# Kernel optimization log

Measured on AMD Instinct MI355X. Metric: run time of the kernel, lower is better.

## Reference

```python
import jax, jax.numpy as jnp
import numpy as np

B, V, D, H = 16, 20000, 256, 256
EPS = 1e-5


def _ln(x, g, b):
    m = jnp.mean(x, axis=-1, keepdims=True)
    v = jnp.mean(jnp.square(x - m), axis=-1, keepdims=True)
    return (x - m) * jax.lax.rsqrt(v + EPS) * g + b


def setup_inputs() -> dict:
    key = jax.random.key(0)
    ks = jax.random.split(key, 8)
    s = 1.0 / np.sqrt(D)
    return {
        "patient_emb": jax.random.normal(ks[0], (B, D), jnp.float32),
        "atc4_emb_matrix": jax.random.normal(ks[1], (V, D), jnp.float32),
        "Wp": jax.random.normal(ks[2], (D, D), jnp.float32) * s,
        "bp": jnp.zeros((D,), jnp.float32),
        "gp": jnp.ones((D,), jnp.float32),
        "betap": jnp.zeros((D,), jnp.float32),
        "Wa": jax.random.normal(ks[3], (D, D), jnp.float32) * s,
        "ba": jnp.zeros((D,), jnp.float32),
        "ga": jnp.ones((D,), jnp.float32),
        "betaa": jnp.zeros((D,), jnp.float32),
        "W1": jax.random.normal(ks[4], (2 * D, H), jnp.float32) * (1.0 / np.sqrt(2 * D)),
        "b1": jnp.zeros((H,), jnp.float32),
        "W2": jax.random.normal(ks[5], (H,), jnp.float32) * (1.0 / np.sqrt(H)),
        "b2": jnp.zeros((1,), jnp.float32),
        "g_pred": jnp.ones((V,), jnp.float32),
        "b_pred": jnp.zeros((V,), jnp.float32),
    }


def reference(patient_emb, atc4_emb_matrix, Wp, bp, gp, betap, Wa, ba, ga, betaa,
              W1, b1, W2, b2, g_pred, b_pred):
    # patient projector + layernorm: (B, D)
    p = _ln(patient_emb @ Wp + bp, gp, betap)
    # atc4 projector + layernorm: (V, D)
    a = _ln(atc4_emb_matrix @ Wa + ba, ga, betaa)
    # AttentionFusion: concat([p_expand, a_expand], -1) @ W1 == p@W1[:D] + a@W1[D:]
    ph = p @ W1[:D]            # (B, H)
    ah = a @ W1[D:]            # (V, H)
    h = jnp.tanh(ph[:, None, :] + ah[None, :, :] + b1)   # (B, V, H)
    scores = jnp.einsum('bvh,h->bv', h, W2) + b2[0]       # (B, V)
    # pred layernorm over the vocab dimension
    return _ln(scores, g_pred, b_pred)
```

## Files before the change

kernel.cpp:

```cpp
#include <hip/hip_runtime.h>


typedef unsigned short ushort_t;
typedef __attribute__((ext_vector_type(8))) short short8;
typedef __attribute__((ext_vector_type(4))) float floatx4;

#define C2F 2.8853900817779268f
#define V_N 20000
#define NBLK 1250

__device__ __forceinline__ ushort_t f2bf(float f) {
    unsigned int u = __builtin_bit_cast(unsigned int, f);
    u += 0x7FFFu + ((u >> 16) & 1u);
    return (ushort_t)(u >> 16);
}
__device__ __forceinline__ float exp2_fast(float x) { return __builtin_amdgcn_exp2f(x); }
__device__ __forceinline__ float rcp_fast(float x)  { return __builtin_amdgcn_rcpf(x); }

__global__ __launch_bounds__(1024) void prep_kernel(
    const float* __restrict__ patient_emb, const float* __restrict__ Wp,
    const float* __restrict__ bp, const float* __restrict__ gp,
    const float* __restrict__ betap, const float* __restrict__ Wa,
    const float* __restrict__ W1, ushort_t* __restrict__ pWa,
    ushort_t* __restrict__ pW1b, float* __restrict__ EpT)
{
    const int blk = blockIdx.x;
    const int tid = threadIdx.x;
    __shared__ float peL[256];
    __shared__ float pL[256];
    __shared__ float part[4][256];
    __shared__ float red[8];

    if (blk < 16) {
        int slot = blk * 1024 + tid;
        int matrix = slot >> 13;
        int rest = slot & 8191;
        int s = rest >> 10, T = (rest >> 6) & 15, l = rest & 63;
        const float* src = matrix ? (W1 + 256 * 256) : Wa;
        ushort_t* dst = matrix ? pW1b : pWa;
        int kbase = s * 32 + ((l >> 4) << 3);
        int nn = (T << 4) + (l & 15);
        short8 t;
        #pragma unroll
        for (int j = 0; j < 8; ++j)
            t[j] = (short)f2bf(src[(kbase + j) * 256 + nn]);
        *(short8*)(dst + rest * 8) = t;
        return;
    }

    const int b = blk - 16;
    const int j = tid & 255, pq = tid >> 8;
    if (tid < 256) peL[tid] = patient_emb[b * 256 + tid];
    __syncthreads();
    float a0 = 0.f;
    #pragma unroll 8
    for (int dd = 0; dd < 64; ++dd) {
        int d = pq * 64 + dd;
        a0 += peL[d] * Wp[d * 256 + j];
    }
    part[pq][j] = a0;
    __syncthreads();
    float x = 0.f;
    if (tid < 256) {
        x = part[0][j] + part[1][j] + part[2][j] + part[3][j] + bp[j];
        float s1 = x, s2 = x * x;
        #pragma unroll
        for (int off = 32; off; off >>= 1) {
            s1 += __shfl_xor(s1, off);
            s2 += __shfl_xor(s2, off);
        }
        int wv = tid >> 6;
        if ((tid & 63) == 0) { red[wv * 2] = s1; red[wv * 2 + 1] = s2; }
    }
    __syncthreads();
    if (tid < 256) {
        float s1 = red[0] + red[2] + red[4] + red[6];
        float s2 = red[1] + red[3] + red[5] + red[7];
        float mean = s1 * (1.f / 256.f);
        float var  = s2 * (1.f / 256.f) - mean * mean;
        float rstd = rsqrtf(var + 1e-5f);
        pL[tid] = (x - mean) * rstd * gp[tid] + betap[tid];
    }
    __syncthreads();
    float a2 = 0.f;
    #pragma unroll 8
    for (int dd = 0; dd < 64; ++dd) {
        int d = pq * 64 + dd;
        a2 += pL[d] * W1[d * 256 + j];
    }
    part[pq][j] = a2;
    __syncthreads();
    if (tid < 256)
        EpT[tid * 16 + b] = exp2_fast(
            C2F * (part[0][tid] + part[1][tid] + part[2][tid] + part[3][tid]));
}

__global__ __launch_bounds__(256, 3) void mega_kernel(
    const float* __restrict__ atc4, const float* __restrict__ ba,
    const float* __restrict__ ga, const float* __restrict__ betaa,
    const float* __restrict__ b1, const float* __restrict__ W2,
    const ushort_t* __restrict__ pWa, const ushort_t* __restrict__ pW1b,
    const float* __restrict__ EpT, float* __restrict__ scores,
    float* __restrict__ s1g, float* __restrict__ s2g)
{
    __shared__ ushort_t AtileF[4096];
    __shared__ float EpL[256 * 20];
    __shared__ float statsP[4][16][2];
    __shared__ float statsF[16][2];
    __shared__ float redbuf[16][4][17];

    const int tid = threadIdx.x;
    const int w = tid >> 6, lane = tid & 63;
    const int q = lane >> 4, n = lane & 15;
    const int v0 = blockIdx.x * 16;

    #pragma unroll
    for (int i = 0; i < 16; ++i) {
        int idx = i * 256 + tid;
        EpL[(idx >> 4) * 20 + (idx & 15)] = EpT[idx];
    }
    {
        const int row = tid >> 4;
        const int kb = (tid & 15) * 16;
        const float* srcp = atc4 + (v0 + row) * 256 + kb;
        #pragma unroll
        for (int i = 0; i < 4; ++i) {
            int k = kb + i * 4;
            float4 f = *(const float4*)(srcp + i * 4);
            ushort4 usv = make_ushort4(f2bf(f.x), f2bf(f.y), f2bf(f.z), f2bf(f.w));
            int addr = (((k >> 5) * 64) + (((k >> 3) & 3) * 16) + row) * 8 + (k & 7);
            *(ushort4*)(AtileF + addr) = usv;
        }
    }
    __syncthreads();

    floatx4 acc[4];
    #pragma unroll
    for (int ni = 0; ni < 4; ++ni) acc[ni] = (floatx4){0.f, 0.f, 0.f, 0.f};
    #pragma unroll
    for (int s = 0; s < 8; ++s) {
        short8 a0 = ((const short8*)AtileF)[s * 64 + lane];
        #pragma unroll
        for (int ni = 0; ni < 4; ++ni) {
            short8 bfv = *(const short8*)(pWa + ((s * 16 + w * 4 + ni) * 64 + lane) * 8);
            acc[ni] = __builtin_amdgcn_mfma_f32_16x16x32_bf16(a0, bfv, acc[ni], 0, 0, 0);
        }
    }

    float bac[4], gac[4], bec[4], b1c[4], w2c[4];
    #pragma unroll
    for (int ni = 0; ni < 4; ++ni) {
        int col = w * 64 + ni * 16 + n;
        bac[ni] = ba[col]; gac[ni] = ga[col]; bec[ni] = betaa[col];
        b1c[ni] = C2F * b1[col]; w2c[ni] = W2[col];
    }

    float s1v[4] = {0, 0, 0, 0}, s2v[4] = {0, 0, 0, 0};
    #pragma unroll
    for (int ni = 0; ni < 4; ++ni)
        #pragma unroll
        for (int r = 0; r < 4; ++r) {
            float x = acc[ni][r] + bac[ni];
            acc[ni][r] = x;
            s1v[r] += x; s2v[r] += x * x;
        }
    #pragma unroll
    for (int off = 1; off < 16; off <<= 1)
        #pragma unroll
        for (int r = 0; r < 4; ++r) {
            s1v[r] += __shfl_xor(s1v[r], off);
            s2v[r] += __shfl_xor(s2v[r], off);
        }
    if (n == 0) {
        #pragma unroll
        for (int r = 0; r < 4; ++r) {
            statsP[w][q * 4 + r][0] = s1v[r];
            statsP[w][q * 4 + r][1] = s2v[r];
        }
    }
    __syncthreads();
    if (tid < 16) {
        float m1 = statsP[0][tid][0] + statsP[1][tid][0] + statsP[2][tid][0] + statsP[3][tid][0];
        float m2 = statsP[0][tid][1] + statsP[1][tid][1] + statsP[2][tid][1] + statsP[3][tid][1];
        float mean = m1 * (1.f / 256.f);
        float var  = m2 * (1.f / 256.f) - mean * mean;
        statsF[tid][0] = mean;
        statsF[tid][1] = rsqrtf(var + 1e-5f);
    }
    __syncthreads();

    #pragma unroll
    for (int r = 0; r < 4; ++r) {
        int row = q * 4 + r;
        float mean = statsF[row][0], rstd = statsF[row][1];
        #pragma unroll
        for (int ni = 0; ni < 4; ++ni) {
            float xv = (acc[ni][r] - mean) * rstd * gac[ni] + bec[ni];
            int addr = ((w * 2 + (ni >> 1)) * 64 +
                        ((ni & 1) * 2 + (n >> 3)) * 16 + row) * 8 + (n & 7);
            AtileF[addr] = f2bf(xv);
        }
    }
    __syncthreads();

    floatx4 acc2[4];
    #pragma unroll
    for (int ni = 0; ni < 4; ++ni) acc2[ni] = (floatx4){0.f, 0.f, 0.f, 0.f};
    #pragma unroll
    for (int s = 0; s < 8; ++s) {
        short8 a0 = ((const short8*)AtileF)[s * 64 + lane];
        #pragma unroll
        for (int ni = 0; ni < 4; ++ni) {
            short8 bfv = *(const short8*)(pW1b + ((s * 16 + w * 4 + ni) * 64 + lane) * 8);
            acc2[ni] = __builtin_amdgcn_mfma_f32_16x16x32_bf16(a0, bfv, acc2[ni], 0, 0, 0);
        }
    }

    #pragma unroll
    for (int ni = 0; ni < 4; ++ni)
        #pragma unroll
        for (int r = 0; r < 4; ++r)
            acc2[ni][r] = exp2_fast(fmaf(C2F, acc2[ni][r], b1c[ni]));

    #pragma unroll 1
    for (int p = 0; p < 4; ++p) {
        float accs[4][4];
        #pragma unroll
        for (int bb = 0; bb < 4; ++bb)
            #pragma unroll
            for (int r = 0; r < 4; ++r) accs[bb][r] = 0.f;
        #pragma unroll
        for (int ni = 0; ni < 4; ++ni) {
            int base = (w * 64 + ni * 16 + n) * 20 + p * 4;
            float4 e0 = *(const float4*)(&EpL[base]);
            float ep[4] = {e0.x, e0.y, e0.z, e0.w};
            #pragma unroll
            for (int bb = 0; bb < 4; ++bb)
                #pragma unroll
                for (int r = 0; r < 4; ++r)
                    accs[bb][r] += w2c[ni] * rcp_fast(fmaf(ep[bb], acc2[ni][r], 1.f));
        }
        float t2v[2][4], t1[4];
        {
            int hb = n & 1;
            #pragma unroll
            for (int p2 = 0; p2 < 2; ++p2)
                #pragma unroll
                for (int r = 0; r < 4; ++r) {
                    float keep = hb ? accs[2 * p2 + 1][r] : accs[2 * p2][r];
                    float send = hb ? accs[2 * p2][r] : accs[2 * p2 + 1][r];
                    t2v[p2][r] = keep + __shfl_xor(send, 1);
                }
            hb = (n >> 1) & 1;
            #pragma unroll
            for (int r = 0; r < 4; ++r) {
                float keep = hb ? t2v[1][r] : t2v[0][r];
                float send = hb ? t2v[0][r] : t2v[1][r];
                t1[r] = keep + __shfl_xor(send, 2);
            }
            #pragma unroll
            for (int r = 0; r < 4; ++r) {
                t1[r] += __shfl_xor(t1[r], 4);
                t1[r] += __shfl_xor(t1[r], 8);
            }
        }
        if (n < 4) {
            #pragma unroll
            for (int r = 0; r < 4; ++r)
                redbuf[p * 4 + n][w][q * 4 + r] = t1[r];
        }
    }
    __syncthreads();
    {
        int bb = tid >> 4, v = tid & 15;
        float S = redbuf[bb][0][v] + redbuf[bb][1][v] +
                  redbuf[bb][2][v] + redbuf[bb][3][v];
        scores[bb * V_N + v0 + v] = S;
        float ls1 = S, ls2 = S * S;
        #pragma unroll
        for (int off = 1; off < 16; off <<= 1) {
            ls1 += __shfl_xor(ls1, off);
            ls2 += __shfl_xor(ls2, off);
        }
        if ((tid & 15) == 0) {
            s1g[bb * NBLK + blockIdx.x] = ls1;
            s2g[bb * NBLK + blockIdx.x] = ls2;
        }
    }
}

__global__ __launch_bounds__(256) void final_kernel(
    const float* __restrict__ scores, const float* __restrict__ s1g,
    const float* __restrict__ s2g, const float* __restrict__ g_pred,
    const float* __restrict__ b_pred, float* __restrict__ out)
{
    const int cx = blockIdx.x, b = blockIdx.y, tid = threadIdx.x;
    __shared__ float redL[8];
    float ls1 = 0.f, ls2 = 0.f;
    for (int i = tid; i < NBLK; i += 256) {
        ls1 += s1g[b * NBLK + i];
        ls2 += s2g[b * NBLK + i];
    }
    #pragma unroll
    for (int off = 32; off; off >>= 1) {
        ls1 += __shfl_xor(ls1, off);
        ls2 += __shfl_xor(ls2, off);
    }
    int w = tid >> 6;
    if ((tid & 63) == 0) { redL[w] = ls1; redL[4 + w] = ls2; }
    __syncthreads();
    float S1 = redL[0] + redL[1] + redL[2] + redL[3];
    float S2 = redL[4] + redL[5] + redL[6] + redL[7];
    float mean = S1 * (1.f / 20000.f);
    float var  = S2 * (1.f / 20000.f) - mean * mean;
    float k = -2.f * rsqrtf(4.f * var + 1e-5f);
    #pragma unroll
    for (int i = 0; i < 8; ++i) {
        int off = i * 256 + tid;
        if (off < 2000) {
            int v = cx * 2000 + off;
            float S = scores[b * V_N + v];
            out[b * V_N + v] = (S - mean) * k * g_pred[v] + b_pred[v];
        }
    }
}

extern "C" void kernel_launch(void* const* d_in, const int* in_sizes, int n_in,
                              void* d_out, int out_size, void* d_ws, size_t ws_size,
                              hipStream_t stream)
{
    const float* patient_emb = (const float*)d_in[0];
    const float* atc4        = (const float*)d_in[1];
    const float* Wp     = (const float*)d_in[2];
    const float* bp     = (const float*)d_in[3];
    const float* gp     = (const float*)d_in[4];
    const float* betap  = (const float*)d_in[5];
    const float* Wa     = (const float*)d_in[6];
    const float* ba     = (const float*)d_in[7];
    const float* ga     = (const float*)d_in[8];
    const float* betaa  = (const float*)d_in[9];
    const float* W1     = (const float*)d_in[10];
    const float* b1     = (const float*)d_in[11];
    const float* W2     = (const float*)d_in[12];
    const float* g_pred = (const float*)d_in[14];
    const float* b_pred = (const float*)d_in[15];

    char* ws = (char*)d_ws;
    float*    EpT    = (float*)(ws);
    ushort_t* pWa    = (ushort_t*)(ws + 16384);
    ushort_t* pW1b   = (ushort_t*)(ws + 147456);
    float*    scores = (float*)(ws + 278528);
    float*    s1g    = (float*)(ws + 1558528);
    float*    s2g    = (float*)(ws + 1638528);
    float*    out    = (float*)d_out;

    prep_kernel<<<32, 1024, 0, stream>>>(patient_emb, Wp, bp, gp, betap,
                                         Wa, W1, pWa, pW1b, EpT);
    mega_kernel<<<NBLK, 256, 0, stream>>>(atc4, ba, ga, betaa, b1, W2,
                                          pWa, pW1b, EpT, scores, s1g, s2g);
    final_kernel<<<dim3(10, 16), 256, 0, stream>>>(scores, s1g, s2g,
                                                   g_pred, b_pred, out);
}
```

Baseline: 133.6 us.

## Restructure mega kernel into single-wave tile kernel per 16 vocab rows

Replaces the 4-wave 256-thread block with a 64-thread block where one wave computes all 256 output columns for its 16 vocab rows. This removes the cross-wave LDS reductions and most __syncthreads, keeps the first GEMM's A operand in registers, and reads EpT straight from global instead of staging it in LDS. The trade-off is heavy register pressure (two 16-entry floatx4 accumulator sets), only 1250 single-wave blocks, and four times more serial MFMA and tanh work per wave, which may reduce latency hiding.

After: 152.8 us. +14.3%, slower.

```diff
diff --git a/kernel.cpp b/kernel.cpp
--- a/kernel.cpp
+++ b/kernel.cpp
@@ -95,7 +95,7 @@
             C2F * (part[0][tid] + part[1][tid] + part[2][tid] + part[3][tid]));
 }
 
-__global__ __launch_bounds__(256, 3) void mega_kernel(
+__global__ __launch_bounds__(64, 2) void tile_kernel(
     const float* __restrict__ atc4, const float* __restrict__ ba,
     const float* __restrict__ ga, const float* __restrict__ betaa,
     const float* __restrict__ b1, const float* __restrict__ W2,
@@ -103,67 +103,49 @@
     const float* __restrict__ EpT, float* __restrict__ scores,
     float* __restrict__ s1g, float* __restrict__ s2g)
 {
-    __shared__ ushort_t AtileF[4096];
-    __shared__ float EpL[256 * 20];
-    __shared__ float statsP[4][16][2];
-    __shared__ float statsF[16][2];
-    __shared__ float redbuf[16][4][17];
-
-    const int tid = threadIdx.x;
-    const int w = tid >> 6, lane = tid & 63;
+    __shared__ ushort_t Atile2[4096 + 128];
+
+    const int lane = threadIdx.x;
     const int q = lane >> 4, n = lane & 15;
     const int v0 = blockIdx.x * 16;
 
-    #pragma unroll
-    for (int i = 0; i < 16; ++i) {
-        int idx = i * 256 + tid;
-        EpL[(idx >> 4) * 20 + (idx & 15)] = EpT[idx];
-    }
-    {
-        const int row = tid >> 4;
-        const int kb = (tid & 15) * 16;
-        const float* srcp = atc4 + (v0 + row) * 256 + kb;
-        #pragma unroll
-        for (int i = 0; i < 4; ++i) {
-            int k = kb + i * 4;
-            float4 f = *(const float4*)(srcp + i * 4);
-            ushort4 usv = make_ushort4(f2bf(f.x), f2bf(f.y), f2bf(f.z), f2bf(f.w));
-            int addr = (((k >> 5) * 64) + (((k >> 3) & 3) * 16) + row) * 8 + (k & 7);
-            *(ushort4*)(AtileF + addr) = usv;
-        }
-    }
-    __syncthreads();
-
-    floatx4 acc[4];
-    #pragma unroll
-    for (int ni = 0; ni < 4; ++ni) acc[ni] = (floatx4){0.f, 0.f, 0.f, 0.f};
+    short8 af[8];
     #pragma unroll
     for (int s = 0; s < 8; ++s) {
-        short8 a0 = ((const short8*)AtileF)[s * 64 + lane];
-        #pragma unroll
-        for (int ni = 0; ni < 4; ++ni) {
-            short8 bfv = *(const short8*)(pWa + ((s * 16 + w * 4 + ni) * 64 + lane) * 8);
-            acc[ni] = __builtin_amdgcn_mfma_f32_16x16x32_bf16(a0, bfv, acc[ni], 0, 0, 0);
-        }
-    }
-
-    float bac[4], gac[4], bec[4], b1c[4], w2c[4];
-    #pragma unroll
-    for (int ni = 0; ni < 4; ++ni) {
-        int col = w * 64 + ni * 16 + n;
-        bac[ni] = ba[col]; gac[ni] = ga[col]; bec[ni] = betaa[col];
-        b1c[ni] = C2F * b1[col]; w2c[ni] = W2[col];
+        const float* src = atc4 + (v0 + n) * 256 + s * 32 + q * 8;
+        float4 f0 = *(const float4*)(src);
+        float4 f1 = *(const float4*)(src + 4);
+        short8 t;
+        t[0] = (short)f2bf(f0.x); t[1] = (short)f2bf(f0.y);
+        t[2] = (short)f2bf(f0.z); t[3] = (short)f2bf(f0.w);
+        t[4] = (short)f2bf(f1.x); t[5] = (short)f2bf(f1.y);
+        t[6] = (short)f2bf(f1.z); t[7] = (short)f2bf(f1.w);
+        af[s] = t;
+    }
+
+    floatx4 acc[16];
+    #pragma unroll
+    for (int ni = 0; ni < 16; ++ni) acc[ni] = (floatx4){0.f, 0.f, 0.f, 0.f};
+    #pragma unroll
+    for (int s = 0; s < 8; ++s) {
+        #pragma unroll
+        for (int ni = 0; ni < 16; ++ni) {
+            short8 bfv = *(const short8*)(pWa + ((s * 16 + ni) * 64 + lane) * 8);
+            acc[ni] = __builtin_amdgcn_mfma_f32_16x16x32_bf16(af[s], bfv, acc[ni], 0, 0, 0);
+        }
     }
 
     float s1v[4] = {0, 0, 0, 0}, s2v[4] = {0, 0, 0, 0};
     #pragma unroll
-    for (int ni = 0; ni < 4; ++ni)
+    for (int ni = 0; ni < 16; ++ni) {
+        float bav = ba[ni * 16 + n];
         #pragma unroll
         for (int r = 0; r < 4; ++r) {
-            float x = acc[ni][r] + bac[ni];
+            float x = acc[ni][r] + bav;
             acc[ni][r] = x;
             s1v[r] += x; s2v[r] += x * x;
         }
+    }
     #pragma unroll
     for (int off = 1; off < 16; off <<= 1)
         #pragma unroll
@@ -171,57 +153,49 @@
             s1v[r] += __shfl_xor(s1v[r], off);
             s2v[r] += __shfl_xor(s2v[r], off);
         }
-    if (n == 0) {
+    float mean[4], rstd[4];
+    #pragma unroll
+    for (int r = 0; r < 4; ++r) {
+        mean[r] = s1v[r] * (1.f / 256.f);
+        float var = s2v[r] * (1.f / 256.f) - mean[r] * mean[r];
+        rstd[r] = rsqrtf(var + 1e-5f);
+    }
+
+    #pragma unroll
+    for (int ni = 0; ni < 16; ++ni) {
+        float gav = ga[ni * 16 + n], bev = betaa[ni * 16 + n];
         #pragma unroll
         for (int r = 0; r < 4; ++r) {
-            statsP[w][q * 4 + r][0] = s1v[r];
-            statsP[w][q * 4 + r][1] = s2v[r];
-        }
-    }
-    __syncthreads();
-    if (tid < 16) {
-        float m1 = statsP[0][tid][0] + statsP[1][tid][0] + statsP[2][tid][0] + statsP[3][tid][0];
-        float m2 = statsP[0][tid][1] + statsP[1][tid][1] + statsP[2][tid][1] + statsP[3][tid][1];
-        float mean = m1 * (1.f / 256.f);
-        float var  = m2 * (1.f / 256.f) - mean * mean;
-        statsF[tid][0] = mean;
-        statsF[tid][1] = rsqrtf(var + 1e-5f);
-    }
-    __syncthreads();
-
-    #pragma unroll
-    for (int r = 0; r < 4; ++r) {
-        int row = q * 4 + r;
-        float mean = statsF[row][0], rstd = statsF[row][1];
-        #pragma unroll
-        for (int ni = 0; ni < 4; ++ni) {
-            float xv = (acc[ni][r] - mean) * rstd * gac[ni] + bec[ni];
-            int addr = ((w * 2 + (ni >> 1)) * 64 +
-                        ((ni & 1) * 2 + (n >> 3)) * 16 + row) * 8 + (n & 7);
-            AtileF[addr] = f2bf(xv);
-        }
-    }
-    __syncthreads();
-
-    floatx4 acc2[4];
-    #pragma unroll
-    for (int ni = 0; ni < 4; ++ni) acc2[ni] = (floatx4){0.f, 0.f, 0.f, 0.f};
+            float xv = (acc[ni][r] - mean[r]) * rstd[r] * gav + bev;
+            int addr = ((ni >> 1) * 64 + ((ni & 1) * 2 + (n >> 3)) * 16 +
+                        (q * 4 + r)) * 8 + (n & 7);
+            Atile2[addr] = f2bf(xv);
+        }
+    }
+    __syncthreads();
+
+    floatx4 acc2[16];
+    #pragma unroll
+    for (int ni = 0; ni < 16; ++ni) acc2[ni] = (floatx4){0.f, 0.f, 0.f, 0.f};
     #pragma unroll
     for (int s = 0; s < 8; ++s) {
-        short8 a0 = ((const short8*)AtileF)[s * 64 + lane];
-        #pragma unroll
-        for (int ni = 0; ni < 4; ++ni) {
-            short8 bfv = *(const short8*)(pW1b + ((s * 16 + w * 4 + ni) * 64 + lane) * 8);
-            acc2[ni] = __builtin_amdgcn_mfma_f32_16x16x32_bf16(a0, bfv, acc2[ni], 0, 0, 0);
-        }
-    }
-
-    #pragma unroll
-    for (int ni = 0; ni < 4; ++ni)
+        short8 a2 = ((const short8*)Atile2)[s * 64 + lane];
+        #pragma unroll
+        for (int ni = 0; ni < 16; ++ni) {
+            short8 bfv = *(const short8*)(pW1b + ((s * 16 + ni) * 64 + lane) * 8);
+            acc2[ni] = __builtin_amdgcn_mfma_f32_16x16x32_bf16(a2, bfv, acc2[ni], 0, 0, 0);
+        }
+    }
+
+    #pragma unroll
+    for (int ni = 0; ni < 16; ++ni) {
+        float b1v = C2F * b1[ni * 16 + n];
         #pragma unroll
         for (int r = 0; r < 4; ++r)
-            acc2[ni][r] = exp2_fast(fmaf(C2F, acc2[ni][r], b1c[ni]));
-
+            acc2[ni][r] = exp2_fast(fmaf(C2F, acc2[ni][r], b1v));
+    }
+
+    const int blk = blockIdx.x;
     #pragma unroll 1
     for (int p = 0; p < 4; ++p) {
         float accs[4][4];
@@ -230,15 +204,15 @@
             #pragma unroll
             for (int r = 0; r < 4; ++r) accs[bb][r] = 0.f;
         #pragma unroll
-        for (int ni = 0; ni < 4; ++ni) {
-            int base = (w * 64 + ni * 16 + n) * 20 + p * 4;
-            float4 e0 = *(const float4*)(&EpL[base]);
+        for (int ni = 0; ni < 16; ++ni) {
+            float w2v = W2[ni * 16 + n];
+            float4 e0 = *(const float4*)(EpT + (ni * 16 + n) * 16 + p * 4);
             float ep[4] = {e0.x, e0.y, e0.z, e0.w};
             #pragma unroll
             for (int bb = 0; bb < 4; ++bb)
                 #pragma unroll
                 for (int r = 0; r < 4; ++r)
-                    accs[bb][r] += w2c[ni] * rcp_fast(fmaf(ep[bb], acc2[ni][r], 1.f));
+                    accs[bb][r] += w2v * rcp_fast(fmaf(ep[bb], acc2[ni][r], 1.f));
         }
         float t2v[2][4], t1[4];
         {
@@ -265,26 +239,16 @@
             }
         }
         if (n < 4) {
-            #pragma unroll
-            for (int r = 0; r < 4; ++r)
-                redbuf[p * 4 + n][w][q * 4 + r] = t1[r];
-        }
-    }
-    __syncthreads();
-    {
-        int bb = tid >> 4, v = tid & 15;
-        float S = redbuf[bb][0][v] + redbuf[bb][1][v] +
-                  redbuf[bb][2][v] + redbuf[bb][3][v];
-        scores[bb * V_N + v0 + v] = S;
-        float ls1 = S, ls2 = S * S;
-        #pragma unroll
-        for (int off = 1; off < 16; off <<= 1) {
-            ls1 += __shfl_xor(ls1, off);
-            ls2 += __shfl_xor(ls2, off);
-        }
-        if ((tid & 15) == 0) {
-            s1g[bb * NBLK + blockIdx.x] = ls1;
-            s2g[bb * NBLK + blockIdx.x] = ls2;
+            *(float4*)(scores + (p * 4 + n) * V_N + v0 + q * 4) =
+                make_float4(t1[0], t1[1], t1[2], t1[3]);
+        }
+        float ls1 = t1[0] + t1[1] + t1[2] + t1[3];
+        float ls2 = t1[0] * t1[0] + t1[1] * t1[1] + t1[2] * t1[2] + t1[3] * t1[3];
+        ls1 += __shfl_xor(ls1, 16); ls1 += __shfl_xor(ls1, 32);
+        ls2 += __shfl_xor(ls2, 16); ls2 += __shfl_xor(ls2, 32);
+        if (lane < 4) {
+            s1g[(p * 4 + lane) * NBLK + blk] = ls1;
+            s2g[(p * 4 + lane) * NBLK + blk] = ls2;
         }
     }
 }
@@ -356,8 +320,8 @@
 
     prep_kernel<<<32, 1024, 0, stream>>>(patient_emb, Wp, bp, gp, betap,
                                          Wa, W1, pWa, pW1b, EpT);
-    mega_kernel<<<NBLK, 256, 0, stream>>>(atc4, ba, ga, betaa, b1, W2,
-                                          pWa, pW1b, EpT, scores, s1g, s2g);
+    tile_kernel<<<NBLK, 64, 0, stream>>>(atc4, ba, ga, betaa, b1, W2,
+                                         pWa, pW1b, EpT, scores, s1g, s2g);
     final_kernel<<<dim3(10, 16), 256, 0, stream>>>(scores, s1g, s2g,
                                                    g_pred, b_pred, out);
 }
```
